# Kernel optimization log

Hardware: AMD Instinct MI355X
Metric: run time of the kernel (lower is better)

Reference implementation:

```python
import jax, jax.numpy as jnp
import numpy as np

DECAY = 0.99


def setup_inputs() -> dict:
    key = jax.random.key(0)
    k1, k2, k3 = jax.random.split(key, 3)
    B, L, D, N = 8, 2048, 512, 1024
    x = jax.random.normal(k1, (B, L, D), dtype=jnp.float32)
    codebook = jax.random.normal(k2, (N, D), dtype=jnp.float32)
    ema_weight = jax.random.normal(k3, (N, D), dtype=jnp.float32)
    counts = jnp.ones((N,), dtype=jnp.float32)
    return {"x": x, "codebook": codebook, "ema_weight": ema_weight, "counts": counts}


def reference(x, codebook, ema_weight, counts):
    # x: [B, L, D]; codebook/ema_weight: [N, D]; counts: [N]
    n_tokens = codebook.shape[0]
    # avoids materializing the [B,L,N,D] difference tensor of the naive form)
    x_sq = jnp.sum(x * x, axis=-1, keepdims=True)            # [B, L, 1]
    c_sq = jnp.sum(codebook * codebook, axis=-1)             # [N]
    xc = jnp.einsum('bld,nd->bln', x, codebook)              # [B, L, N]
    distances = jnp.sqrt(jnp.maximum(x_sq - 2.0 * xc + c_sq, 0.0))
    indices = jnp.argmin(distances, axis=-1)                 # [B, L]
    encodings = jax.nn.one_hot(indices, n_tokens, dtype=jnp.float32)  # [B, L, N]
    # train=True branch: EMA codebook update
    counts_new = DECAY * counts + (1.0 - DECAY) * jnp.sum(encodings, axis=(0, 1))
    dw = jnp.einsum('bln,bld->nd', encodings, x)             # [N, D]
    ema_new = DECAY * ema_weight + (1.0 - DECAY) * dw
    codebook_new = ema_new / counts_new[:, None]
    # quantization with straight-through estimator
    quantized = jnp.einsum('bln,nd->bld', encodings, codebook_new)  # [B, L, D]
    quantized = x + jax.lax.stop_gradient(quantized - x)
    # optax.l2_loss(x, quantized) = 0.5 * (x - quantized)^2
    codebook_loss = jnp.mean(0.5 * jnp.square(x - quantized))
    return quantized, codebook_loss, indices
```

## Files before the change

### kernel.cpp

```cpp
#include <hip/hip_runtime.h>
#include <hip/hip_bf16.h>

constexpr int Dd   = 512;
constexpr int Nn   = 1024;
constexpr int Ttok = 16384;
constexpr float DECAYc = 0.99f;
constexpr float GAP = 3.0f;
constexpr int CH = 16;

typedef short bf16x8 __attribute__((ext_vector_type(8)));
typedef float f32x4  __attribute__((ext_vector_type(4)));
typedef unsigned short us8v __attribute__((ext_vector_type(8)));

__device__ inline unsigned short f2bf(float f) {
  unsigned int b = __float_as_uint(f);
  return (unsigned short)((b + 0x7FFFu + ((b >> 16) & 1u)) >> 16);
}
__device__ inline unsigned cvtpk(float lo, float hi) {
  unsigned r;
  asm("v_cvt_pk_bf16_f32 %0, %1, %2" : "=v"(r) : "v"(lo), "v"(hi));
  return r;
}

__global__ __launch_bounds__(64) void k_prep_cb(const float* __restrict__ cb,
                                                unsigned short* __restrict__ cbh,
                                                float* __restrict__ csq) {
  const int n = blockIdx.x, l = threadIdx.x;
  const float4* r = (const float4*)(cb + (size_t)n * Dd);
  float4 a = r[l], b = r[l + 64];
  float ss = a.x*a.x + a.y*a.y + a.z*a.z + a.w*a.w
           + b.x*b.x + b.y*b.y + b.z*b.z + b.w*b.w;
  ushort4 ua, ub;
  ua.x = f2bf(a.x); ua.y = f2bf(a.y); ua.z = f2bf(a.z); ua.w = f2bf(a.w);
  ub.x = f2bf(b.x); ub.y = f2bf(b.y); ub.z = f2bf(b.z); ub.w = f2bf(b.w);
  ((ushort4*)(cbh + (size_t)n * Dd))[l]      = ua;
  ((ushort4*)(cbh + (size_t)n * Dd))[l + 64] = ub;
#pragma unroll
  for (int o = 32; o; o >>= 1) ss += __shfl_down(ss, o);
  if (l == 0) csq[n] = ss;
}

__global__ __launch_bounds__(256) void k_gemm_scores(
    const unsigned short* __restrict__ cbh, const float* __restrict__ x,
    const float* __restrict__ csq, float4* __restrict__ part) {
  __shared__ unsigned short As[2][128 * 64];
  __shared__ unsigned short Bs[128 * 64];
  const int tid = threadIdx.x;
  const int w = tid >> 6, l = tid & 63;
  const int b = blockIdx.x;
  const int s = (b & 7) * 128 + (b >> 3);
  const int cm = s & 7;
  const int tn = s >> 3;
  const int wr = w >> 1, wc = w & 1;

  const int srow = tid >> 3;
  const int xorw = (tid >> 3) & 7;
  const int scolA = ((tid & 7) ^ xorw) * 8;
  const int scolB = (tid & 7) * 8;
  const int wcolB = ((tid & 7) ^ xorw) * 8;

  f32x4 acc[4][4] = {};

  const unsigned short* gA0 = cbh + (size_t)(cm * 128) * Dd;
  const float*          gB0 = x   + (size_t)(tn * 128) * Dd;

  uint4 bq[4];
#define LOADB(KC) do {                                                        \
    const int k0_ = (KC) * 64;                                                \
    _Pragma("unroll")                                                         \
    for (int p = 0; p < 4; ++p) {                                             \
      const float* gb = gB0 + (size_t)(p * 32 + srow) * Dd + k0_ + scolB;     \
      float4 v0_ = *(const float4*)gb;                                        \
      float4 v1_ = *(const float4*)(gb + 4);                                  \
      bq[p].x = cvtpk(v0_.x, v0_.y); bq[p].y = cvtpk(v0_.z, v0_.w);           \
      bq[p].z = cvtpk(v1_.x, v1_.y); bq[p].w = cvtpk(v1_.z, v1_.w);           \
    }                                                                         \
  } while (0)
#define ISSUEA(KC, BUF) do {                                                  \
    const int k0_ = (KC) * 64;                                                \
    _Pragma("unroll")                                                         \
    for (int c = 0; c < 4; ++c) {                                             \
      const unsigned short* ga = gA0 + (size_t)(c * 32 + srow) * Dd + k0_ + scolA; \
      char* la = (char*)&As[BUF][0] + c * 4096 + w * 1024;                    \
      __builtin_amdgcn_global_load_lds((const __attribute__((address_space(1))) void*)ga, \
                                       (__attribute__((address_space(3))) void*)la, 16, 0, 0); \
    }                                                                         \
  } while (0)

  ISSUEA(0, 0);
  LOADB(0);

  for (int kc = 0; kc < Dd / 64; ++kc) {
    __syncthreads();
#pragma unroll
    for (int p = 0; p < 4; ++p)
      *(uint4*)&Bs[(p * 32 + srow) * 64 + wcolB] = bq[p];
    __syncthreads();
    if (kc + 1 < Dd / 64) {
      ISSUEA(kc + 1, (kc + 1) & 1);
      LOADB(kc + 1);
    }
    const unsigned short* Ab = &As[kc & 1][0];
#pragma unroll
    for (int ks = 0; ks < 2; ++ks) {
      const int ra = l & 15;
      const int rx = l & 7;
      const int kbs = ((ks * 4 + (l >> 4)) ^ rx) * 8;
      bf16x8 af[4], bfr[4];
#pragma unroll
      for (int m = 0; m < 4; ++m)
        af[m] = *(const bf16x8*)&Ab[(wr * 64 + m * 16 + ra) * 64 + kbs];
#pragma unroll
      for (int n = 0; n < 4; ++n)
        bfr[n] = *(const bf16x8*)&Bs[(wc * 64 + n * 16 + ra) * 64 + kbs];
#pragma unroll
      for (int m = 0; m < 4; ++m)
#pragma unroll
        for (int n = 0; n < 4; ++n)
          acc[m][n] = __builtin_amdgcn_mfma_f32_16x16x32_bf16(af[m], bfr[n], acc[m][n], 0, 0, 0);
    }
  }
#undef LOADB
#undef ISSUEA

  const int base4 = wr * 64 + (l >> 4) * 4;
  float4 cs[4];
#pragma unroll
  for (int m = 0; m < 4; ++m)
    cs[m] = *(const float4*)&csq[cm * 128 + base4 + m * 16];

  const int slot = cm * 2 + wr;
  const int tok0 = tn * 128 + wc * 64 + (l & 15);

#pragma unroll
  for (int n = 0; n < 4; ++n) {
    float v0 = 3.4e38f, v1 = 3.4e38f, v2 = 3.4e38f;
    int i0 = 0x7fffffff, i1 = 0x7fffffff;
#pragma unroll
    for (int m = 0; m < 4; ++m) {
#pragma unroll
      for (int r = 0; r < 4; ++r) {
        float sv = fmaf(-2.0f, acc[m][n][r], ((const float*)&cs[m])[r]);
        int idx = cm * 128 + base4 + m * 16 + r;
        if (sv < v0)      { v2 = v1; v1 = v0; i1 = i0; v0 = sv; i0 = idx; }
        else if (sv < v1) { v2 = v1; v1 = sv; i1 = idx; }
        else if (sv < v2) { v2 = sv; }
      }
    }
#pragma unroll
    for (int o = 16; o <= 32; o <<= 1) {
      float w0 = __shfl_xor(v0, o), w1 = __shfl_xor(v1, o), w2 = __shfl_xor(v2, o);
      int  j0 = __shfl_xor(i0, o), j1 = __shfl_xor(i1, o);
      bool f = (w0 < v0) || (w0 == v0 && j0 < i0);
      float A0 = f ? w0 : v0, A1 = f ? w1 : v1, A2 = f ? w2 : v2;
      int  Ai0 = f ? j0 : i0, Ai1 = f ? j1 : i1;
      float B0 = f ? v0 : w0, B1 = f ? v1 : w1;
      int  Bi0 = f ? i0 : j0;
      bool g = (A1 < B0) || (A1 == B0 && Ai1 < Bi0);
      v0 = A0; i0 = Ai0;
      v1 = g ? A1 : B0; i1 = g ? Ai1 : Bi0;
      v2 = g ? fminf(A2, B0) : fminf(A1, B1);
    }
    if ((l >> 4) == 0)
      part[(size_t)slot * Ttok + tok0 + n * 16] = make_float4(
          v0, v1, __uint_as_float((unsigned)i0 | ((unsigned)i1 << 16)), v2);
  }
}

__device__ inline void rescore(int n, const float4& xa, const float4& xb,
                               const float* __restrict__ cb,
                               const float* __restrict__ csq, int l,
                               float& bestv, int& besti) {
  const float4* cr = (const float4*)(cb + (size_t)n * Dd);
  float4 ca = cr[l * 2], cc = cr[l * 2 + 1];
  float p = xa.x*ca.x + xa.y*ca.y + xa.z*ca.z + xa.w*ca.w
          + xb.x*cc.x + xb.y*cc.y + xb.z*cc.z + xb.w*cc.w;
#pragma unroll
  for (int o = 32; o; o >>= 1) p += __shfl_xor(p, o);
  float sc = csq[n] - 2.0f * p;
  if (sc < bestv || (sc == bestv && n < besti)) { bestv = sc; besti = n; }
}

__device__ inline void rescore_half(int h, const float* __restrict__ xrow,
                                    const float* __restrict__ cb,
                                    const float* __restrict__ csq, int l,
                                    float& bestv, int& besti) {
  int n = h * 64 + l;
  const float4* cr = (const float4*)(cb + (size_t)n * Dd);
  const float4* xr = (const float4*)xrow;
  float p = 0.f;
#pragma unroll 8
  for (int j = 0; j < 128; ++j) {
    float4 c4 = cr[j], x4 = xr[j];
    p += c4.x*x4.x + c4.y*x4.y + c4.z*x4.z + c4.w*x4.w;
  }
  float sc = csq[n] - 2.0f * p;
#pragma unroll
  for (int o = 1; o < 64; o <<= 1) {
    float ov = __shfl_xor(sc, o); int oi = __shfl_xor(n, o);
    if (ov < sc || (ov == sc && oi < n)) { sc = ov; n = oi; }
  }
  if (sc < bestv || (sc == bestv && n < besti)) { bestv = sc; besti = n; }
}

__global__ __launch_bounds__(256) void k_select(
    const float4* __restrict__ part, const float* __restrict__ x,
    const float* __restrict__ cb, const float* __restrict__ csq,
    int* __restrict__ idxb, float* __restrict__ idxf, float* __restrict__ hist) {
  const int tid = threadIdx.x, wid = tid >> 6, l = tid & 63;
  const int t = blockIdx.x * 4 + wid;
  float v0 = 3.4e38f, v1 = 3.4e38f, v2 = 3.4e38f;
  int i0 = 0x7fffffff, i1 = 0x7fffffff;
  if (l < 16) {
    float4 e = part[(size_t)l * Ttok + t];
    v0 = e.x; v1 = e.y; v2 = e.w;
    unsigned ii = __float_as_uint(e.z);
    i0 = (int)(ii & 0xffff); i1 = (int)(ii >> 16);
  }
  float A0 = v0, A1 = v1; int Ai0 = i0, Ai1 = i1;
#pragma unroll
  for (int o = 1; o < 16; o <<= 1) {
    float w0 = __shfl_xor(A0, o), w1 = __shfl_xor(A1, o);
    int  j0 = __shfl_xor(Ai0, o), j1 = __shfl_xor(Ai1, o);
    bool f = (w0 < A0) || (w0 == A0 && j0 < Ai0);
    float B0 = f ? A0 : w0; int Bi0 = f ? Ai0 : j0;
    float W1 = f ? w1 : A1; int Wi1 = f ? j1 : Ai1;
    if (f) { A0 = w0; Ai0 = j0; }
    bool g = (B0 < W1) || (B0 == W1 && Bi0 < Wi1);
    A1 = g ? B0 : W1; Ai1 = g ? Bi0 : Wi1;
  }
  const float m  = __shfl(A0, 0);
  const float g1 = __shfl(A1, 0);
  const int   gi = __shfl(Ai0, 0);
  int besti;
  if (g1 - m > GAP) {
    besti = gi;
  } else {
    const float thr = m + GAP;
    const float* xrow = x + (size_t)t * Dd;
    const float4* xr = (const float4*)xrow;
    float4 xa = xr[l * 2], xb = xr[l * 2 + 1];
    float bestv = 3.4e38f; besti = 0x7fffffff;
    for (int h = 0; h < 16; ++h) {
      float b0 = __shfl(v0, h);
      if (b0 > thr) continue;
      float b1 = __shfl(v1, h), b2 = __shfl(v2, h);
      int bi0 = __shfl(i0, h), bi1 = __shfl(i1, h);
      if (b2 <= thr) {
        rescore_half(h, xrow, cb, csq, l, bestv, besti);
      } else {
        rescore(bi0, xa, xb, cb, csq, l, bestv, besti);
        if (b1 <= thr) rescore(bi1, xa, xb, cb, csq, l, bestv, besti);
      }
    }
  }
  if (l == 0) {
    idxb[t] = besti;
    idxf[t] = (float)besti;
    atomicAdd(&hist[besti], 1.0f);
  }
}

__global__ __launch_bounds__(256) void k_offsets(const float* __restrict__ hist,
                                                 int* __restrict__ offs,
                                                 int* __restrict__ cursor) {
  __shared__ int wsum[4];
  const int tid = threadIdx.x, l = tid & 63, wd = tid >> 6;
  const int base = tid * 4;
  int c0 = (int)hist[base], c1 = (int)hist[base + 1],
      c2 = (int)hist[base + 2], c3 = (int)hist[base + 3];
  int sum = c0 + c1 + c2 + c3;
  int sc = sum;
#pragma unroll
  for (int o = 1; o < 64; o <<= 1) { int v = __shfl_up(sc, o); if (l >= o) sc += v; }
  if (l == 63) wsum[wd] = sc;
  __syncthreads();
  int wbase = 0;
  for (int i = 0; i < wd; ++i) wbase += wsum[i];
  int e = wbase + sc - sum;
  offs[base] = e;     cursor[base] = e;
  offs[base+1] = e + c0; cursor[base+1] = e + c0;
  offs[base+2] = e + c0 + c1; cursor[base+2] = e + c0 + c1;
  offs[base+3] = e + c0 + c1 + c2; cursor[base+3] = e + c0 + c1 + c2;
}

__global__ __launch_bounds__(256) void k_scatter(const int* __restrict__ idxb,
                                                 int* __restrict__ cursor,
                                                 int* __restrict__ bucket,
                                                 int* __restrict__ bcode) {
  int t = blockIdx.x * 256 + threadIdx.x;
  if (t < Ttok) {
    int n = idxb[t];
    int p = atomicAdd(&cursor[n], 1);
    bucket[p] = t;
    bcode[p] = n;
  }
}

__global__ __launch_bounds__(512) void k_dw_part(
    const float* __restrict__ x, const int* __restrict__ bucket,
    const int* __restrict__ bcode, float* __restrict__ dw) {
  __shared__ int sh_t[CH], sh_n[CH];
  const int tid = threadIdx.x;
  const int p0 = blockIdx.x * CH;
  if (tid < CH) { sh_t[tid] = bucket[p0 + tid]; sh_n[tid] = bcode[p0 + tid]; }
  __syncthreads();
  float v[CH];
#pragma unroll
  for (int j = 0; j < CH; ++j)
    v[j] = x[(size_t)sh_t[j] * Dd + tid];
  float acc = v[0]; int cur = sh_n[0];
#pragma unroll
  for (int j = 1; j < CH; ++j) {
    int n = sh_n[j];
    if (n != cur) { atomicAdd(&dw[(size_t)cur * Dd + tid], acc); acc = 0.f; cur = n; }
    acc += v[j];
  }
  atomicAdd(&dw[(size_t)cur * Dd + tid], acc);
}

__global__ __launch_bounds__(256) void finalize_cb(
    const float* __restrict__ ema, const float* __restrict__ dw,
    const float* __restrict__ counts, const float* __restrict__ hist,
    float* __restrict__ cbnew) {
  int e4 = blockIdx.x * 256 + threadIdx.x;
  int n = e4 >> 7;
  float cnt = DECAYc * counts[n] + (1.0f - DECAYc) * hist[n];
  float inv = 1.0f / cnt;
  float4 e = ((const float4*)ema)[e4];
  float4 d = ((const float4*)dw)[e4];
  float4 o;
  o.x = (DECAYc * e.x + (1.0f - DECAYc) * d.x) * inv;
  o.y = (DECAYc * e.y + (1.0f - DECAYc) * d.y) * inv;
  o.z = (DECAYc * e.z + (1.0f - DECAYc) * d.z) * inv;
  o.w = (DECAYc * e.w + (1.0f - DECAYc) * d.w) * inv;
  ((float4*)cbnew)[e4] = o;
}

__global__ __launch_bounds__(256) void quant_loss(
    const float* __restrict__ x, const float* __restrict__ cbnew,
    const int* __restrict__ idx, float* __restrict__ out_q,
    float* __restrict__ loss) {
  const int e0 = blockIdx.x * 256 + threadIdx.x;
  const int gsz = 524288;
  int n[4]; float4 q[4], xv[4];
#pragma unroll
  for (int j = 0; j < 4; ++j) n[j] = idx[(e0 + j * gsz) >> 7];
#pragma unroll
  for (int j = 0; j < 4; ++j) {
    const int e = e0 + j * gsz;
    q[j]  = ((const float4*)(cbnew + (size_t)n[j] * Dd))[e & 127];
    xv[j] = ((const float4*)x)[e];
  }
  float part = 0.f;
#pragma unroll
  for (int j = 0; j < 4; ++j) {
    ((float4*)out_q)[e0 + j * gsz] = q[j];
    float dx = xv[j].x - q[j].x, dy = xv[j].y - q[j].y,
          dz = xv[j].z - q[j].z, dw_ = xv[j].w - q[j].w;
    part += dx*dx + dy*dy + dz*dz + dw_*dw_;
  }
  __shared__ float red[4];
#pragma unroll
  for (int o = 32; o; o >>= 1) part += __shfl_down(part, o);
  int wid = threadIdx.x >> 6, lane = threadIdx.x & 63;
  if (lane == 0) red[wid] = part;
  __syncthreads();
  if (threadIdx.x == 0) atomicAdd(loss, red[0] + red[1] + red[2] + red[3]);
}

__global__ void loss_final(const float* __restrict__ loss,
                           float* __restrict__ out_loss) {
  *out_loss = loss[0] * (0.5f / (float)((size_t)Ttok * Dd));
}

extern "C" void kernel_launch(void* const* d_in, const int* in_sizes, int n_in,
                              void* d_out, int out_size, void* d_ws, size_t ws_size,
                              hipStream_t stream) {
  const float* x      = (const float*)d_in[0];
  const float* cb     = (const float*)d_in[1];
  const float* ema    = (const float*)d_in[2];
  const float* counts = (const float*)d_in[3];

  float* out      = (float*)d_out;
  float* q_out    = out;
  float* loss_out = out + (size_t)Ttok * Dd;
  float* idxf_out = loss_out + 1;
  float4* part = (float4*)q_out;

  float* ws = (float*)d_ws;
  unsigned short* cbh = (unsigned short*)ws;
  float* dw      = ws + 262144;
  float* hist    = ws + 786432;
  float* loss    = ws + 787456;
  float* csq     = ws + 787460;
  int*   offs    = (int*)(ws + 788484);
  int*   cursor  = (int*)(ws + 789508);
  int*   bucket  = (int*)(ws + 790532);
  int*   bcode   = (int*)(ws + 806916);
  int*   idxb    = (int*)(ws + 823300);
  float* cbnew   = ws + 839684;

  hipMemsetAsync(dw, 0, (size_t)525316 * sizeof(float), stream);

  k_prep_cb<<<Nn, 64, 0, stream>>>(cb, cbh, csq);
  k_gemm_scores<<<(Nn / 128) * (Ttok / 128), 256, 0, stream>>>(cbh, x, csq, part);
  k_select<<<Ttok / 4, 256, 0, stream>>>(part, x, cb, csq, idxb, idxf_out, hist);
  k_offsets<<<1, 256, 0, stream>>>(hist, offs, cursor);
  k_scatter<<<Ttok / 256, 256, 0, stream>>>(idxb, cursor, bucket, bcode);
  k_dw_part<<<Ttok / CH, 512, 0, stream>>>(x, bucket, bcode, dw);
  finalize_cb<<<(Nn * Dd / 4) / 256, 256, 0, stream>>>(ema, dw, counts, hist, cbnew);
  quant_loss<<<2048, 256, 0, stream>>>(x, cbnew, idxb, q_out, loss);
  loss_final<<<1, 1, 0, stream>>>(loss, loss_out);
}
```

Measured before the change: 131.6 us.

## Pre-convert x to bf16 once and load both GEMM operands via direct-to-LDS

Adds a combined prep kernel that converts the codebook and x to bf16 and zeroes the workspace, replacing the memset and the separate codebook prep launch. The x bf16 copy sits in the unused upper half of the quantized output buffer. The scores GEMM now double-buffers both operands in LDS with global_load_lds and drops the per-tile register-staged fp32 conversion and one barrier per k-step. This removes eight-fold redundant fp32 reads and conversions of x across codebook tiles. It adds one extra pass over x and uses twice the LDS for B, and the quant_loss output stores are made nontemporal.

New measurement: 124.5 us. 5.4% less time.

```diff
diff --git a/kernel.cpp b/kernel.cpp
--- a/kernel.cpp
+++ b/kernel.cpp
@@ -10,41 +10,58 @@
 
 typedef short bf16x8 __attribute__((ext_vector_type(8)));
 typedef float f32x4  __attribute__((ext_vector_type(4)));
-typedef unsigned short us8v __attribute__((ext_vector_type(8)));
-
-__device__ inline unsigned short f2bf(float f) {
-  unsigned int b = __float_as_uint(f);
-  return (unsigned short)((b + 0x7FFFu + ((b >> 16) & 1u)) >> 16);
-}
+
 __device__ inline unsigned cvtpk(float lo, float hi) {
   unsigned r;
   asm("v_cvt_pk_bf16_f32 %0, %1, %2" : "=v"(r) : "v"(lo), "v"(hi));
   return r;
 }
 
-__global__ __launch_bounds__(64) void k_prep_cb(const float* __restrict__ cb,
-                                                unsigned short* __restrict__ cbh,
-                                                float* __restrict__ csq) {
-  const int n = blockIdx.x, l = threadIdx.x;
-  const float4* r = (const float4*)(cb + (size_t)n * Dd);
-  float4 a = r[l], b = r[l + 64];
-  float ss = a.x*a.x + a.y*a.y + a.z*a.z + a.w*a.w
-           + b.x*b.x + b.y*b.y + b.z*b.z + b.w*b.w;
-  ushort4 ua, ub;
-  ua.x = f2bf(a.x); ua.y = f2bf(a.y); ua.z = f2bf(a.z); ua.w = f2bf(a.w);
-  ub.x = f2bf(b.x); ub.y = f2bf(b.y); ub.z = f2bf(b.z); ub.w = f2bf(b.w);
-  ((ushort4*)(cbh + (size_t)n * Dd))[l]      = ua;
-  ((ushort4*)(cbh + (size_t)n * Dd))[l + 64] = ub;
-#pragma unroll
-  for (int o = 32; o; o >>= 1) ss += __shfl_down(ss, o);
-  if (l == 0) csq[n] = ss;
+constexpr int NB_CB = 256, NB_Z = 32, NB_X = 2048;
+constexpr int ZF4 = 131329;
+__global__ __launch_bounds__(256) void k_prep(
+    const float* __restrict__ cb, const float* __restrict__ x,
+    unsigned short* __restrict__ cbh, float* __restrict__ csq,
+    unsigned short* __restrict__ xh, float4* __restrict__ zbase) {
+  const int b = blockIdx.x, tid = threadIdx.x;
+  if (b < NB_CB) {
+    const int n = b * 4 + (tid >> 6), l = tid & 63;
+    const float4* r = (const float4*)(cb + (size_t)n * Dd);
+    float4 a = r[l], c = r[l + 64];
+    float ss = a.x*a.x + a.y*a.y + a.z*a.z + a.w*a.w
+             + c.x*c.x + c.y*c.y + c.z*c.z + c.w*c.w;
+    uint2 ua, uc;
+    ua.x = cvtpk(a.x, a.y); ua.y = cvtpk(a.z, a.w);
+    uc.x = cvtpk(c.x, c.y); uc.y = cvtpk(c.z, c.w);
+    ((uint2*)(cbh + (size_t)n * Dd))[l]      = ua;
+    ((uint2*)(cbh + (size_t)n * Dd))[l + 64] = uc;
+#pragma unroll
+    for (int o = 32; o; o >>= 1) ss += __shfl_down(ss, o);
+    if (l == 0) csq[n] = ss;
+  } else if (b < NB_CB + NB_Z) {
+    const float4 z = make_float4(0.f, 0.f, 0.f, 0.f);
+    for (int i = (b - NB_CB) * 256 + tid; i < ZF4; i += NB_Z * 256)
+      zbase[i] = z;
+  } else {
+    const int bx = b - (NB_CB + NB_Z);
+#pragma unroll
+    for (int k = 0; k < 2; ++k) {
+      const int i = bx * 512 + k * 256 + tid;
+      float4 a = ((const float4*)x)[i * 2];
+      float4 c = ((const float4*)x)[i * 2 + 1];
+      uint4 o;
+      o.x = cvtpk(a.x, a.y); o.y = cvtpk(a.z, a.w);
+      o.z = cvtpk(c.x, c.y); o.w = cvtpk(c.z, c.w);
+      ((uint4*)xh)[i] = o;
+    }
+  }
 }
 
 __global__ __launch_bounds__(256) void k_gemm_scores(
-    const unsigned short* __restrict__ cbh, const float* __restrict__ x,
+    const unsigned short* __restrict__ cbh, const unsigned short* __restrict__ xh,
     const float* __restrict__ csq, float4* __restrict__ part) {
   __shared__ unsigned short As[2][128 * 64];
-  __shared__ unsigned short Bs[128 * 64];
+  __shared__ unsigned short Bs[2][128 * 64];
   const int tid = threadIdx.x;
   const int w = tid >> 6, l = tid & 63;
   const int b = blockIdx.x;
@@ -55,52 +72,35 @@
 
   const int srow = tid >> 3;
   const int xorw = (tid >> 3) & 7;
-  const int scolA = ((tid & 7) ^ xorw) * 8;
-  const int scolB = (tid & 7) * 8;
-  const int wcolB = ((tid & 7) ^ xorw) * 8;
+  const int scol = ((tid & 7) ^ xorw) * 8;
 
   f32x4 acc[4][4] = {};
 
   const unsigned short* gA0 = cbh + (size_t)(cm * 128) * Dd;
-  const float*          gB0 = x   + (size_t)(tn * 128) * Dd;
-
-  uint4 bq[4];
-#define LOADB(KC) do {                                                        \
-    const int k0_ = (KC) * 64;                                                \
-    _Pragma("unroll")                                                         \
-    for (int p = 0; p < 4; ++p) {                                             \
-      const float* gb = gB0 + (size_t)(p * 32 + srow) * Dd + k0_ + scolB;     \
-      float4 v0_ = *(const float4*)gb;                                        \
-      float4 v1_ = *(const float4*)(gb + 4);                                  \
-      bq[p].x = cvtpk(v0_.x, v0_.y); bq[p].y = cvtpk(v0_.z, v0_.w);           \
-      bq[p].z = cvtpk(v1_.x, v1_.y); bq[p].w = cvtpk(v1_.z, v1_.w);           \
-    }                                                                         \
-  } while (0)
-#define ISSUEA(KC, BUF) do {                                                  \
+  const unsigned short* gB0 = xh  + (size_t)(tn * 128) * Dd;
+
+#define ISSUE(KC, BUF) do {                                                   \
     const int k0_ = (KC) * 64;                                                \
     _Pragma("unroll")                                                         \
     for (int c = 0; c < 4; ++c) {                                             \
-      const unsigned short* ga = gA0 + (size_t)(c * 32 + srow) * Dd + k0_ + scolA; \
+      const unsigned short* ga = gA0 + (size_t)(c * 32 + srow) * Dd + k0_ + scol; \
+      const unsigned short* gb = gB0 + (size_t)(c * 32 + srow) * Dd + k0_ + scol; \
       char* la = (char*)&As[BUF][0] + c * 4096 + w * 1024;                    \
+      char* lb = (char*)&Bs[BUF][0] + c * 4096 + w * 1024;                    \
       __builtin_amdgcn_global_load_lds((const __attribute__((address_space(1))) void*)ga, \
                                        (__attribute__((address_space(3))) void*)la, 16, 0, 0); \
+      __builtin_amdgcn_global_load_lds((const __attribute__((address_space(1))) void*)gb, \
+                                       (__attribute__((address_space(3))) void*)lb, 16, 0, 0); \
     }                                                                         \
   } while (0)
 
-  ISSUEA(0, 0);
-  LOADB(0);
+  ISSUE(0, 0);
 
   for (int kc = 0; kc < Dd / 64; ++kc) {
     __syncthreads();
-#pragma unroll
-    for (int p = 0; p < 4; ++p)
-      *(uint4*)&Bs[(p * 32 + srow) * 64 + wcolB] = bq[p];
-    __syncthreads();
-    if (kc + 1 < Dd / 64) {
-      ISSUEA(kc + 1, (kc + 1) & 1);
-      LOADB(kc + 1);
-    }
+    if (kc + 1 < Dd / 64) ISSUE(kc + 1, (kc + 1) & 1);
     const unsigned short* Ab = &As[kc & 1][0];
+    const unsigned short* Bb = &Bs[kc & 1][0];
 #pragma unroll
     for (int ks = 0; ks < 2; ++ks) {
       const int ra = l & 15;
@@ -112,7 +112,7 @@
         af[m] = *(const bf16x8*)&Ab[(wr * 64 + m * 16 + ra) * 64 + kbs];
 #pragma unroll
       for (int n = 0; n < 4; ++n)
-        bfr[n] = *(const bf16x8*)&Bs[(wc * 64 + n * 16 + ra) * 64 + kbs];
+        bfr[n] = *(const bf16x8*)&Bb[(wc * 64 + n * 16 + ra) * 64 + kbs];
 #pragma unroll
       for (int m = 0; m < 4; ++m)
 #pragma unroll
@@ -120,8 +120,7 @@
           acc[m][n] = __builtin_amdgcn_mfma_f32_16x16x32_bf16(af[m], bfr[n], acc[m][n], 0, 0, 0);
     }
   }
-#undef LOADB
-#undef ISSUEA
+#undef ISSUE
 
   const int base4 = wr * 64 + (l >> 4) * 4;
   float4 cs[4];
@@ -343,22 +342,21 @@
     float* __restrict__ loss) {
   const int e0 = blockIdx.x * 256 + threadIdx.x;
   const int gsz = 524288;
-  int n[4]; float4 q[4], xv[4];
+  int n[4]; f32x4 q[4], xv[4];
 #pragma unroll
   for (int j = 0; j < 4; ++j) n[j] = idx[(e0 + j * gsz) >> 7];
 #pragma unroll
   for (int j = 0; j < 4; ++j) {
     const int e = e0 + j * gsz;
-    q[j]  = ((const float4*)(cbnew + (size_t)n[j] * Dd))[e & 127];
-    xv[j] = ((const float4*)x)[e];
+    q[j]  = ((const f32x4*)(cbnew + (size_t)n[j] * Dd))[e & 127];
+    xv[j] = ((const f32x4*)x)[e];
   }
   float part = 0.f;
 #pragma unroll
   for (int j = 0; j < 4; ++j) {
-    ((float4*)out_q)[e0 + j * gsz] = q[j];
-    float dx = xv[j].x - q[j].x, dy = xv[j].y - q[j].y,
-          dz = xv[j].z - q[j].z, dw_ = xv[j].w - q[j].w;
-    part += dx*dx + dy*dy + dz*dz + dw_*dw_;
+    __builtin_nontemporal_store(q[j], &((f32x4*)out_q)[e0 + j * gsz]);
+    f32x4 d = xv[j] - q[j];
+    part += d[0]*d[0] + d[1]*d[1] + d[2]*d[2] + d[3]*d[3];
   }
   __shared__ float red[4];
 #pragma unroll
@@ -387,6 +385,7 @@
   float* loss_out = out + (size_t)Ttok * Dd;
   float* idxf_out = loss_out + 1;
   float4* part = (float4*)q_out;
+  unsigned short* xh = (unsigned short*)(q_out + 2097152);
 
   float* ws = (float*)d_ws;
   unsigned short* cbh = (unsigned short*)ws;
@@ -401,10 +400,8 @@
   int*   idxb    = (int*)(ws + 823300);
   float* cbnew   = ws + 839684;
 
-  hipMemsetAsync(dw, 0, (size_t)525316 * sizeof(float), stream);
-
-  k_prep_cb<<<Nn, 64, 0, stream>>>(cb, cbh, csq);
-  k_gemm_scores<<<(Nn / 128) * (Ttok / 128), 256, 0, stream>>>(cbh, x, csq, part);
+  k_prep<<<NB_CB + NB_Z + NB_X, 256, 0, stream>>>(cb, x, cbh, csq, xh, (float4*)dw);
+  k_gemm_scores<<<(Nn / 128) * (Ttok / 128), 256, 0, stream>>>(cbh, xh, csq, part);
   k_select<<<Ttok / 4, 256, 0, stream>>>(part, x, cb, csq, idxb, idxf_out, hist);
   k_offsets<<<1, 256, 0, stream>>>(hist, offs, cursor);
   k_scatter<<<Ttok / 256, 256, 0, stream>>>(idxb, cursor, bucket, bcode);
```
